# Performance work log

Measured on AMD Instinct MI355X. Metric: run time of the kernel, lower is better.

Reference implementation:

```python
import jax, jax.numpy as jnp
import numpy as np

NUM_NODES = 2048
EMB = (512, 512, 256)
LATENT = 512
N_FEAT = 512
N_TOTAL = 16384  # batch_size * NUM_NODES
N_EDGES = 524288


def setup_inputs() -> dict:
    key = jax.random.key(0)
    ks = jax.random.split(key, 14)
    s = 0.02
    inp = {
        "x": jax.random.normal(ks[0], (N_TOTAL, N_FEAT), jnp.float32),
        "edge_index": jax.random.randint(ks[1], (2, N_EDGES), 0, N_TOTAL, dtype=jnp.int64),
        "batch_size": 8,
        "batch_index": jax.random.randint(ks[2], (N_TOTAL,), 0, 8, dtype=jnp.int64),
        "W1": jax.random.normal(ks[3], (N_FEAT, EMB[0]), jnp.float32) * s,
        "b1": jnp.zeros((EMB[0],), jnp.float32),
        "W2": jax.random.normal(ks[4], (EMB[0], EMB[1]), jnp.float32) * s,
        "b2": jnp.zeros((EMB[1],), jnp.float32),
        "W3": jax.random.normal(ks[5], (EMB[1], EMB[2]), jnp.float32) * s,
        "b3": jnp.zeros((EMB[2],), jnp.float32),
        "We": jax.random.normal(ks[6], (NUM_NODES * EMB[2], LATENT), jnp.float32) * s,
        "be": jnp.zeros((LATENT,), jnp.float32),
        "Wd": jax.random.normal(ks[7], (LATENT, NUM_NODES), jnp.float32) * s,
        "bd": jnp.zeros((NUM_NODES,), jnp.float32),
    }
    return inp


def reference(x, edge_index, batch_size, batch_index, W1, b1, W2, b2, W3, b3, We, be, Wd, bd):
    N = x.shape[0]
    loops = jnp.arange(N)
    row = jnp.concatenate([edge_index[0], loops])  # sources
    col = jnp.concatenate([edge_index[1], loops])  # targets
    # symmetric degree normalization (PyG GCNConv with self loops)
    deg = jax.ops.segment_sum(jnp.ones_like(col, dtype=x.dtype), col, num_segments=N)
    dinv = jnp.where(deg > 0, jax.lax.rsqrt(deg), jnp.zeros_like(deg))
    norm = (dinv[row] * dinv[col])[:, None]  # [E+N, 1]

    def gcn(h, W, b):
        h = h @ W  # transform first (PyG order)
        return jax.ops.segment_sum(h[row] * norm, col, num_segments=N) + b

    h = jax.nn.relu(gcn(x, W1, b1))
    h = jax.nn.relu(gcn(h, W2, b2))
    h = gcn(h, W3, b3)                      # [N, EMB[2]]
    h = h.reshape(-1, NUM_NODES * EMB[2])   # [batch, NUM_NODES*EMB[2]]
    z = h @ We + be                          # encoder Linear
    out = z @ Wd + bd                        # decoder Linear -> [batch, NUM_NODES]
    return out
```

## Files before the change

kernel.cpp:

```cpp
#include <hip/hip_runtime.h>
#include <stdint.h>

#define NT 16384
#define NN 2048
#define NB 8

typedef __attribute__((ext_vector_type(4))) float f32x4;
typedef __attribute__((ext_vector_type(2))) float f32x2;
typedef __attribute__((ext_vector_type(8))) short s16x8;
typedef __attribute__((ext_vector_type(4))) short s16x4;

__device__ __forceinline__ float bf2f(short u) {
    unsigned v = ((unsigned)(unsigned short)u) << 16;
    return __builtin_bit_cast(float, v);
}
__device__ __forceinline__ short f2bf(float f) {
    unsigned u = __builtin_bit_cast(unsigned, f);
    u += 0x7fffu + ((u >> 16) & 1u);
    return (short)(u >> 16);
}
__device__ __forceinline__ void gload16(const void* g, void* l) {
    __builtin_amdgcn_global_load_lds(
        (const __attribute__((address_space(1))) void*)g,
        (__attribute__((address_space(3))) void*)l, 16, 0, 0);
}
__device__ __forceinline__ long long eidx(const void* ei, long long i, int is64) {
    if (is64) return ((const long long*)ei)[i];
    return (long long)((const int*)ei)[i];
}

__global__ void k_detect(const void* ei, int nchk, int* flag) {
    __shared__ int bad;
    if (threadIdx.x == 0) bad = 0;
    __syncthreads();
    const long long* p = (const long long*)ei;
    for (int i = threadIdx.x; i < nchk; i += 256) {
        long long v = p[i];
        if (v < 0 || v >= NT) bad = 1;
    }
    __syncthreads();
    if (threadIdx.x == 0) *flag = bad ? 0 : 1;
}

__global__ void k_count(const void* ei, int E, const int* flag, int* count) {
    int e = blockIdx.x * 256 + threadIdx.x;
    if (e >= E) return;
    int f = *flag;
    int c = (int)eidx(ei, (long long)E + e, f);
    atomicAdd(&count[c], 1);
}

__global__ __launch_bounds__(1024) void k_scan(const int* __restrict__ count,
        int* __restrict__ offs, float* __restrict__ dinv) {
    __shared__ int ps[1024];
    const int t = threadIdx.x;
    const int base = t * 16;
    int loc[16];
    int s = 0;
#pragma unroll
    for (int j = 0; j < 16; j++) { loc[j] = count[base + j]; s += loc[j]; }
    ps[t] = s;
    __syncthreads();
    for (int o = 1; o < 1024; o <<= 1) {
        int v = (t >= o) ? ps[t - o] : 0;
        __syncthreads();
        ps[t] += v;
        __syncthreads();
    }
    int ex = ps[t] - s;
#pragma unroll
    for (int j = 0; j < 16; j++) {
        offs[base + j] = ex;
        ex += loc[j];
        dinv[base + j] = rsqrtf((float)(loc[j] + 1));
    }
}

__global__ void k_fill(const void* ei, int E, const int* flag,
                       const int* offs, int* cursor, int* csr) {
    int e = blockIdx.x * 256 + threadIdx.x;
    if (e >= E) return;
    int f = *flag;
    int r = (int)eidx(ei, e, f);
    int c = (int)eidx(ei, (long long)E + e, f);
    int pos = offs[c] + atomicAdd(&cursor[c], 1);
    csr[pos] = r;
}

__global__ void k_convw_all(const float* __restrict__ W1, const float* __restrict__ W2,
                            const float* __restrict__ W3, short* __restrict__ Wt1,
                            short* __restrict__ Wt2, short* __restrict__ Wt3) {
    int idx = blockIdx.x * 256 + threadIdx.x;
    const float* W; short* Wt; int N, base;
    if (idx < 262144)      { W = W1; Wt = Wt1; N = 512; base = idx; }
    else if (idx < 524288) { W = W2; Wt = Wt2; N = 512; base = idx - 262144; }
    else                   { W = W3; Wt = Wt3; N = 256; base = idx - 524288; }
    int k = base / N, n = base - k * N;
    Wt[(size_t)n * 512 + k] = f2bf(W[base]);
}

__global__ __launch_bounds__(256) void k_scale_x(const float* __restrict__ x,
        const float* __restrict__ dinv, short* __restrict__ xs) {
    int i = blockIdx.x * 256 + threadIdx.x;
    f32x4 v = *(const f32x4*)(x + (size_t)i * 4);
    float d = dinv[i >> 7];
    s16x4 o;
#pragma unroll
    for (int j = 0; j < 4; j++) o[j] = f2bf(v[j] * d);
    *(s16x4*)(xs + (size_t)i * 4) = o;
}

__global__ __launch_bounds__(256) void k_gemm(const short* __restrict__ A,
        const short* __restrict__ Bt, short* __restrict__ Co, int N, int K) {
    __shared__ short As[4096];
    __shared__ short Bs[4096];
    const int t = threadIdx.x;
    const int w = t >> 6, l = t & 63;
    const int row0 = blockIdx.x * 128;
    const int col0 = blockIdx.y * 128;
    const int lr = l & 15, lhi = l >> 4;
    const int wr = (w >> 1) * 64, wc = (w & 1) * 64;
    const int srow = t >> 2;
    const int skoff = (t & 3) * 8;
    const int ldsbase = w * 512;
    f32x4 acc[4][4] = {};
    for (int k0 = 0; k0 < K; k0 += 32) {
#pragma unroll
        for (int i = 0; i < 2; i++) {
            int r = i * 64 + srow;
            gload16(A  + (size_t)(row0 + r) * K + k0 + skoff, (void*)(As + i * 2048 + ldsbase));
            gload16(Bt + (size_t)(col0 + r) * K + k0 + skoff, (void*)(Bs + i * 2048 + ldsbase));
        }
        __syncthreads();
        s16x8 af[4], bfr[4];
#pragma unroll
        for (int m = 0; m < 4; m++) af[m]  = *(const s16x8*)(As + (wr + m * 16 + lr) * 32 + lhi * 8);
#pragma unroll
        for (int n = 0; n < 4; n++) bfr[n] = *(const s16x8*)(Bs + (wc + n * 16 + lr) * 32 + lhi * 8);
#pragma unroll
        for (int m = 0; m < 4; m++)
#pragma unroll
            for (int n = 0; n < 4; n++)
                acc[m][n] = __builtin_amdgcn_mfma_f32_16x16x32_bf16(af[m], bfr[n], acc[m][n], 0, 0, 0);
        __syncthreads();
    }
#pragma unroll
    for (int m = 0; m < 4; m++)
#pragma unroll
        for (int n = 0; n < 4; n++)
#pragma unroll
            for (int j = 0; j < 4; j++) {
                int r = row0 + wr + m * 16 + lhi * 4 + j;
                int c = col0 + wc + n * 16 + lr;
                Co[(size_t)r * N + c] = f2bf(acc[m][n][j]);
            }
}

__global__ __launch_bounds__(256) void k_agg512(const short* __restrict__ T,
        const int* __restrict__ offs, const int* __restrict__ cnt,
        const int* __restrict__ csr, const float* __restrict__ dinv,
        const float* __restrict__ bias, short* __restrict__ H) {
    const int w = threadIdx.x >> 6, l = threadIdx.x & 63;
    const int node = blockIdx.x * 4 + w;
    const int c0 = l * 8;
    const short* base = T + c0;
    float acc[8];
    {
        s16x8 r = *(const s16x8*)(base + (size_t)node * 512);
#pragma unroll
        for (int v = 0; v < 8; v++) acc[v] = bf2f(r[v]);
    }
    const int beg = offs[node], end = beg + cnt[node];
    int j = beg;
    for (; j + 8 <= end; j += 8) {
        int sIx[8];
#pragma unroll
        for (int q = 0; q < 8; q++) sIx[q] = csr[j + q];
        s16x8 r[8];
#pragma unroll
        for (int q = 0; q < 8; q++) r[q] = *(const s16x8*)(base + (size_t)sIx[q] * 512);
#pragma unroll
        for (int v = 0; v < 8; v++) {
            float s01 = bf2f(r[0][v]) + bf2f(r[1][v]);
            float s23 = bf2f(r[2][v]) + bf2f(r[3][v]);
            float s45 = bf2f(r[4][v]) + bf2f(r[5][v]);
            float s67 = bf2f(r[6][v]) + bf2f(r[7][v]);
            acc[v] += (s01 + s23) + (s45 + s67);
        }
    }
    for (; j + 2 <= end; j += 2) {
        int s0 = csr[j], s1 = csr[j + 1];
        s16x8 r0 = *(const s16x8*)(base + (size_t)s0 * 512);
        s16x8 r1 = *(const s16x8*)(base + (size_t)s1 * 512);
#pragma unroll
        for (int v = 0; v < 8; v++) acc[v] += bf2f(r0[v]) + bf2f(r1[v]);
    }
    for (; j < end; j++) {
        s16x8 r0 = *(const s16x8*)(base + (size_t)csr[j] * 512);
#pragma unroll
        for (int v = 0; v < 8; v++) acc[v] += bf2f(r0[v]);
    }
    const float dc = dinv[node];
    f32x4 b0 = *(const f32x4*)(bias + c0);
    f32x4 b1 = *(const f32x4*)(bias + c0 + 4);
    s16x8 outv;
#pragma unroll
    for (int v = 0; v < 8; v++) {
        float bb = (v < 4) ? b0[v] : b1[v - 4];
        float o = acc[v] * dc + bb;
        o = fmaxf(o, 0.f);
        o *= dc;
        outv[v] = f2bf(o);
    }
    *(s16x8*)(H + (size_t)node * 512 + c0) = outv;
}

__global__ __launch_bounds__(256) void k_agg256(const short* __restrict__ T,
        const int* __restrict__ offs, const int* __restrict__ cnt,
        const int* __restrict__ csr, const float* __restrict__ dinv,
        const float* __restrict__ bias, float* __restrict__ H3) {
    const int w = threadIdx.x >> 6, l = threadIdx.x & 63;
    const int node = blockIdx.x * 4 + w;
    const int c0 = l * 4;
    const short* base = T + c0;
    float acc[4];
    {
        s16x4 r = *(const s16x4*)(base + (size_t)node * 256);
#pragma unroll
        for (int v = 0; v < 4; v++) acc[v] = bf2f(r[v]);
    }
    const int beg = offs[node], end = beg + cnt[node];
    int j = beg;
    for (; j + 8 <= end; j += 8) {
        int sIx[8];
#pragma unroll
        for (int q = 0; q < 8; q++) sIx[q] = csr[j + q];
        s16x4 r[8];
#pragma unroll
        for (int q = 0; q < 8; q++) r[q] = *(const s16x4*)(base + (size_t)sIx[q] * 256);
#pragma unroll
        for (int v = 0; v < 4; v++) {
            float s01 = bf2f(r[0][v]) + bf2f(r[1][v]);
            float s23 = bf2f(r[2][v]) + bf2f(r[3][v]);
            float s45 = bf2f(r[4][v]) + bf2f(r[5][v]);
            float s67 = bf2f(r[6][v]) + bf2f(r[7][v]);
            acc[v] += (s01 + s23) + (s45 + s67);
        }
    }
    for (; j < end; j++) {
        s16x4 r0 = *(const s16x4*)(base + (size_t)csr[j] * 256);
#pragma unroll
        for (int v = 0; v < 4; v++) acc[v] += bf2f(r0[v]);
    }
    const float dc = dinv[node];
    f32x4 bb = *(const f32x4*)(bias + c0);
    f32x4 o;
#pragma unroll
    for (int v = 0; v < 4; v++) o[v] = acc[v] * dc + bb[v];
    *(f32x4*)(H3 + (size_t)node * 256 + c0) = o;
}

__global__ __launch_bounds__(256) void k_enc(const float* __restrict__ h3,
        const float* __restrict__ We, float* __restrict__ part) {
    __shared__ float hT[512 * 8];
    __shared__ float red[32 * 128];
    const int t = threadIdx.x;
    const int k0 = blockIdx.x * 512;
    for (int i = t; i < 4096; i += 256) {
        int b = i >> 9, k = i & 511;
        hT[k * 8 + b] = h3[(size_t)b * 524288 + k0 + k];
    }
    __syncthreads();
    const int col = (t & 127) * 4;
    const int khalf = t >> 7;
    float acc[8][4] = {};
    const float* wp = We + (size_t)(k0 + khalf * 256) * 512 + col;
    const float* hp = hT + khalf * 256 * 8;
#pragma unroll 2
    for (int k = 0; k < 256; k++) {
        f32x4 wv = *(const f32x4*)(wp + (size_t)k * 512);
        f32x4 ha = *(const f32x4*)(hp + k * 8);
        f32x4 hb = *(const f32x4*)(hp + k * 8 + 4);
#pragma unroll
        for (int c = 0; c < 4; c++) {
            acc[0][c] += ha[0] * wv[c];
            acc[1][c] += ha[1] * wv[c];
            acc[2][c] += ha[2] * wv[c];
            acc[3][c] += ha[3] * wv[c];
            acc[4][c] += hb[0] * wv[c];
            acc[5][c] += hb[1] * wv[c];
            acc[6][c] += hb[2] * wv[c];
            acc[7][c] += hb[3] * wv[c];
        }
    }
    if (khalf) {
#pragma unroll
        for (int b = 0; b < 8; b++)
#pragma unroll
            for (int c = 0; c < 4; c++)
                red[(b * 4 + c) * 128 + (t - 128)] = acc[b][c];
    }
    __syncthreads();
    if (!khalf) {
#pragma unroll
        for (int b = 0; b < 8; b++) {
            f32x4 o;
#pragma unroll
            for (int c = 0; c < 4; c++) o[c] = acc[b][c] + red[(b * 4 + c) * 128 + t];
            *(f32x4*)(part + (size_t)blockIdx.x * 4096 + b * 512 + col) = o;
        }
    }
}

__global__ __launch_bounds__(256) void k_zred(const float* __restrict__ part,
                                              float* __restrict__ zpart) {
    const int n = blockIdx.x * 256 + threadIdx.x;
    const int p0 = blockIdx.y * 128;
    float s = 0.f;
    for (int q = 0; q < 128; q++) s += part[(size_t)(p0 + q) * 4096 + n];
    zpart[(size_t)blockIdx.y * 4096 + n] = s;
}

__global__ __launch_bounds__(256) void k_dec(const float* __restrict__ zpart,
        const float* __restrict__ be, const float* __restrict__ Wd,
        const float* __restrict__ bd, float* __restrict__ out) {
    __shared__ float zs[512];
    const int b = blockIdx.x >> 3;
    const int n = ((blockIdx.x & 7) << 8) + threadIdx.x;
    for (int i = threadIdx.x; i < 512; i += 256) {
        float s = be[i];
#pragma unroll
        for (int p = 0; p < 8; p++) s += zpart[(size_t)p * 4096 + b * 512 + i];
        zs[i] = s;
    }
    __syncthreads();
    float acc = bd[n];
    for (int k = 0; k < 512; k++) acc += zs[k] * Wd[(size_t)k * 2048 + n];
    out[b * 2048 + n] = acc;
}

extern "C" void kernel_launch(void* const* d_in, const int* in_sizes, int n_in,
                              void* d_out, int out_size, void* d_ws, size_t ws_size,
                              hipStream_t stream) {
    const float* x  = (const float*)d_in[0];
    const void*  ei = d_in[1];
    const float* W1 = (const float*)d_in[4];
    const float* b1 = (const float*)d_in[5];
    const float* W2 = (const float*)d_in[6];
    const float* b2 = (const float*)d_in[7];
    const float* W3 = (const float*)d_in[8];
    const float* b3 = (const float*)d_in[9];
    const float* We = (const float*)d_in[10];
    const float* be = (const float*)d_in[11];
    const float* Wd = (const float*)d_in[12];
    const float* bd = (const float*)d_in[13];
    float* out = (float*)d_out;
    const int E = in_sizes[1] / 2;

    char* ws = (char*)d_ws;
    size_t off = 0;
    auto alloc = [&](size_t bytes) {
        void* p = ws + off;
        off = (off + bytes + 255) & ~(size_t)255;
        return p;
    };
    int*   flag   = (int*)  alloc(4);
    int*   count  = (int*)  alloc((size_t)NT * 4);
    int*   cursor = (int*)  alloc((size_t)NT * 4);
    int*   offs   = (int*)  alloc((size_t)NT * 4);
    float* dinv   = (float*)alloc((size_t)NT * 4);
    int*   csr    = (int*)  alloc((size_t)E * 4);
    short* Wt1    = (short*)alloc((size_t)512 * 512 * 2);
    short* Wt2    = (short*)alloc((size_t)512 * 512 * 2);
    short* Wt3    = (short*)alloc((size_t)256 * 512 * 2);
    short* bufA   = (short*)alloc((size_t)NT * 512 * 2);
    short* bufB   = (short*)alloc((size_t)NT * 512 * 2);
    float* part   = (float*)alloc((size_t)1024 * 4096 * 4);
    float* zpart  = (float*)alloc((size_t)8 * 4096 * 4);

    hipMemsetAsync(count, 0, (size_t)NT * 8, stream);

    k_detect<<<1, 256, 0, stream>>>(ei, 2048, flag);
    k_count<<<(E + 255) / 256, 256, 0, stream>>>(ei, E, flag, count);
    k_scan<<<1, 1024, 0, stream>>>(count, offs, dinv);
    k_fill<<<(E + 255) / 256, 256, 0, stream>>>(ei, E, flag, offs, cursor, csr);

    k_convw_all<<<2560, 256, 0, stream>>>(W1, W2, W3, Wt1, Wt2, Wt3);
    k_scale_x<<<(NT * 512 / 4) / 256, 256, 0, stream>>>(x, dinv, bufA);

    dim3 g1(128, 4);
    k_gemm<<<g1, 256, 0, stream>>>(bufA, Wt1, bufB, 512, 512);
    k_agg512<<<NT / 4, 256, 0, stream>>>(bufB, offs, count, csr, dinv, b1, bufA);
    k_gemm<<<g1, 256, 0, stream>>>(bufA, Wt2, bufB, 512, 512);
    k_agg512<<<NT / 4, 256, 0, stream>>>(bufB, offs, count, csr, dinv, b2, bufA);
    dim3 g3(128, 2);
    k_gemm<<<g3, 256, 0, stream>>>(bufA, Wt3, bufB, 256, 512);
    k_agg256<<<NT / 4, 256, 0, stream>>>(bufB, offs, count, csr, dinv, b3, (float*)bufA);

    k_enc<<<1024, 256, 0, stream>>>((const float*)bufA, We, part);
    dim3 gz(16, 8);
    k_zred<<<gz, 256, 0, stream>>>(part, zpart);
    k_dec<<<64, 256, 0, stream>>>(zpart, be, Wd, bd, out);
}
```

Measured before the change: 533.2 us.

## Slice aggregation by channel and widen GEMM K-tile with swizzled LDS

The GEMM now stages a 64-wide K tile per iteration with an XOR-swizzled LDS layout, which halves the barrier count and is meant to avoid LDS bank conflicts. The aggregation kernels are restructured so each block handles a 64-channel slice of the features, and each wave walks 8 (or 4) nodes doing scalar 2-byte gathers per lane. Block index ordering is meant to put slices of nearby nodes close together for cache locality. The risk is that the scalar 2-byte gathers are much narrower than the previous 16-byte vector loads, and every neighbour index list is now reread once per slice.

```diff
diff --git a/kernel.cpp b/kernel.cpp
--- a/kernel.cpp
+++ b/kernel.cpp
@@ -112,36 +112,54 @@
 
 __global__ __launch_bounds__(256) void k_gemm(const short* __restrict__ A,
         const short* __restrict__ Bt, short* __restrict__ Co, int N, int K) {
-    __shared__ short As[4096];
-    __shared__ short Bs[4096];
+    __shared__ short As[8192];
+    __shared__ short Bs[8192];
     const int t = threadIdx.x;
     const int w = t >> 6, l = t & 63;
     const int row0 = blockIdx.x * 128;
     const int col0 = blockIdx.y * 128;
     const int lr = l & 15, lhi = l >> 4;
     const int wr = (w >> 1) * 64, wc = (w & 1) * 64;
-    const int srow = t >> 2;
-    const int skoff = (t & 3) * 8;
-    const int ldsbase = w * 512;
     f32x4 acc[4][4] = {};
-    for (int k0 = 0; k0 < K; k0 += 32) {
-#pragma unroll
-        for (int i = 0; i < 2; i++) {
-            int r = i * 64 + srow;
-            gload16(A  + (size_t)(row0 + r) * K + k0 + skoff, (void*)(As + i * 2048 + ldsbase));
-            gload16(Bt + (size_t)(col0 + r) * K + k0 + skoff, (void*)(Bs + i * 2048 + ldsbase));
+    int srow[4], jsrc[4];
+#pragma unroll
+    for (int i = 0; i < 4; i++) {
+        int s = t + i * 256;
+        srow[i] = s >> 3;
+        jsrc[i] = (s & 7) ^ (srow[i] & 7);
+    }
+    int aoff[2][4], boff[2][4];
+#pragma unroll
+    for (int kk = 0; kk < 2; kk++) {
+#pragma unroll
+        for (int m = 0; m < 4; m++) {
+            int ar = wr + m * 16 + lr;
+            aoff[kk][m] = ar * 64 + (((kk * 4 + lhi) ^ (ar & 7)) << 3);
+            int br = wc + m * 16 + lr;
+            boff[kk][m] = br * 64 + (((kk * 4 + lhi) ^ (br & 7)) << 3);
+        }
+    }
+    for (int k0 = 0; k0 < K; k0 += 64) {
+#pragma unroll
+        for (int i = 0; i < 4; i++) {
+            int s = t + i * 256;
+            gload16(A  + (size_t)(row0 + srow[i]) * K + k0 + jsrc[i] * 8, (void*)(As + s * 8));
+            gload16(Bt + (size_t)(col0 + srow[i]) * K + k0 + jsrc[i] * 8, (void*)(Bs + s * 8));
         }
         __syncthreads();
-        s16x8 af[4], bfr[4];
-#pragma unroll
-        for (int m = 0; m < 4; m++) af[m]  = *(const s16x8*)(As + (wr + m * 16 + lr) * 32 + lhi * 8);
-#pragma unroll
-        for (int n = 0; n < 4; n++) bfr[n] = *(const s16x8*)(Bs + (wc + n * 16 + lr) * 32 + lhi * 8);
-#pragma unroll
-        for (int m = 0; m < 4; m++)
-#pragma unroll
-            for (int n = 0; n < 4; n++)
-                acc[m][n] = __builtin_amdgcn_mfma_f32_16x16x32_bf16(af[m], bfr[n], acc[m][n], 0, 0, 0);
+#pragma unroll
+        for (int kk = 0; kk < 2; kk++) {
+            s16x8 af[4], bfr[4];
+#pragma unroll
+            for (int m = 0; m < 4; m++) af[m]  = *(const s16x8*)(As + aoff[kk][m]);
+#pragma unroll
+            for (int n = 0; n < 4; n++) bfr[n] = *(const s16x8*)(Bs + boff[kk][n]);
+#pragma unroll
+            for (int m = 0; m < 4; m++)
+#pragma unroll
+                for (int n = 0; n < 4; n++)
+                    acc[m][n] = __builtin_amdgcn_mfma_f32_16x16x32_bf16(af[m], bfr[n], acc[m][n], 0, 0, 0);
+        }
         __syncthreads();
     }
 #pragma unroll
@@ -156,108 +174,73 @@
             }
 }
 
-__global__ __launch_bounds__(256) void k_agg512(const short* __restrict__ T,
+__global__ __launch_bounds__(256) void k_aggs512(const unsigned short* __restrict__ T,
         const int* __restrict__ offs, const int* __restrict__ cnt,
         const int* __restrict__ csr, const float* __restrict__ dinv,
-        const float* __restrict__ bias, short* __restrict__ H) {
+        const float* __restrict__ bias, unsigned short* __restrict__ H) {
+    const int slice = blockIdx.x & 7;
+    const int group = blockIdx.x >> 3;
     const int w = threadIdx.x >> 6, l = threadIdx.x & 63;
-    const int node = blockIdx.x * 4 + w;
-    const int c0 = l * 8;
-    const short* base = T + c0;
-    float acc[8];
-    {
-        s16x8 r = *(const s16x8*)(base + (size_t)node * 512);
-#pragma unroll
-        for (int v = 0; v < 8; v++) acc[v] = bf2f(r[v]);
-    }
-    const int beg = offs[node], end = beg + cnt[node];
-    int j = beg;
-    for (; j + 8 <= end; j += 8) {
-        int sIx[8];
-#pragma unroll
-        for (int q = 0; q < 8; q++) sIx[q] = csr[j + q];
-        s16x8 r[8];
-#pragma unroll
-        for (int q = 0; q < 8; q++) r[q] = *(const s16x8*)(base + (size_t)sIx[q] * 512);
-#pragma unroll
-        for (int v = 0; v < 8; v++) {
-            float s01 = bf2f(r[0][v]) + bf2f(r[1][v]);
-            float s23 = bf2f(r[2][v]) + bf2f(r[3][v]);
-            float s45 = bf2f(r[4][v]) + bf2f(r[5][v]);
-            float s67 = bf2f(r[6][v]) + bf2f(r[7][v]);
-            acc[v] += (s01 + s23) + (s45 + s67);
-        }
-    }
-    for (; j + 2 <= end; j += 2) {
-        int s0 = csr[j], s1 = csr[j + 1];
-        s16x8 r0 = *(const s16x8*)(base + (size_t)s0 * 512);
-        s16x8 r1 = *(const s16x8*)(base + (size_t)s1 * 512);
-#pragma unroll
-        for (int v = 0; v < 8; v++) acc[v] += bf2f(r0[v]) + bf2f(r1[v]);
-    }
-    for (; j < end; j++) {
-        s16x8 r0 = *(const s16x8*)(base + (size_t)csr[j] * 512);
-#pragma unroll
-        for (int v = 0; v < 8; v++) acc[v] += bf2f(r0[v]);
-    }
-    const float dc = dinv[node];
-    f32x4 b0 = *(const f32x4*)(bias + c0);
-    f32x4 b1 = *(const f32x4*)(bias + c0 + 4);
-    s16x8 outv;
-#pragma unroll
-    for (int v = 0; v < 8; v++) {
-        float bb = (v < 4) ? b0[v] : b1[v - 4];
-        float o = acc[v] * dc + bb;
-        o = fmaxf(o, 0.f);
-        o *= dc;
-        outv[v] = f2bf(o);
-    }
-    *(s16x8*)(H + (size_t)node * 512 + c0) = outv;
-}
-
-__global__ __launch_bounds__(256) void k_agg256(const short* __restrict__ T,
+    const int ch = slice * 64 + l;
+    const float bch = bias[ch];
+    const unsigned short* Tc = T + ch;
+    const int nbase = (group * 4 + w) * 8;
+    for (int nn = 0; nn < 8; nn++) {
+        const int node = nbase + nn;
+        float acc = bf2f((short)Tc[(size_t)node * 512]);
+        const int beg = offs[node], deg = cnt[node];
+        int j = 0;
+        for (; j + 8 <= deg; j += 8) {
+            int idx[8];
+#pragma unroll
+            for (int q = 0; q < 8; q++) idx[q] = __builtin_nontemporal_load(&csr[beg + j + q]);
+            float v[8];
+#pragma unroll
+            for (int q = 0; q < 8; q++) v[q] = bf2f((short)Tc[(size_t)idx[q] * 512]);
+            acc += ((v[0] + v[1]) + (v[2] + v[3])) + ((v[4] + v[5]) + (v[6] + v[7]));
+        }
+        for (; j < deg; j++) {
+            int s0 = __builtin_nontemporal_load(&csr[beg + j]);
+            acc += bf2f((short)Tc[(size_t)s0 * 512]);
+        }
+        const float dc = dinv[node];
+        float o = fmaxf(acc * dc + bch, 0.f) * dc;
+        H[(size_t)node * 512 + ch] = (unsigned short)f2bf(o);
+    }
+}
+
+__global__ __launch_bounds__(256) void k_aggs256(const unsigned short* __restrict__ T,
         const int* __restrict__ offs, const int* __restrict__ cnt,
         const int* __restrict__ csr, const float* __restrict__ dinv,
         const float* __restrict__ bias, float* __restrict__ H3) {
+    const int slice = blockIdx.x & 3;
+    const int group = blockIdx.x >> 2;
     const int w = threadIdx.x >> 6, l = threadIdx.x & 63;
-    const int node = blockIdx.x * 4 + w;
-    const int c0 = l * 4;
-    const short* base = T + c0;
-    float acc[4];
-    {
-        s16x4 r = *(const s16x4*)(base + (size_t)node * 256);
-#pragma unroll
-        for (int v = 0; v < 4; v++) acc[v] = bf2f(r[v]);
-    }
-    const int beg = offs[node], end = beg + cnt[node];
-    int j = beg;
-    for (; j + 8 <= end; j += 8) {
-        int sIx[8];
-#pragma unroll
-        for (int q = 0; q < 8; q++) sIx[q] = csr[j + q];
-        s16x4 r[8];
-#pragma unroll
-        for (int q = 0; q < 8; q++) r[q] = *(const s16x4*)(base + (size_t)sIx[q] * 256);
-#pragma unroll
-        for (int v = 0; v < 4; v++) {
-            float s01 = bf2f(r[0][v]) + bf2f(r[1][v]);
-            float s23 = bf2f(r[2][v]) + bf2f(r[3][v]);
-            float s45 = bf2f(r[4][v]) + bf2f(r[5][v]);
-            float s67 = bf2f(r[6][v]) + bf2f(r[7][v]);
-            acc[v] += (s01 + s23) + (s45 + s67);
-        }
-    }
-    for (; j < end; j++) {
-        s16x4 r0 = *(const s16x4*)(base + (size_t)csr[j] * 256);
-#pragma unroll
-        for (int v = 0; v < 4; v++) acc[v] += bf2f(r0[v]);
-    }
-    const float dc = dinv[node];
-    f32x4 bb = *(const f32x4*)(bias + c0);
-    f32x4 o;
-#pragma unroll
-    for (int v = 0; v < 4; v++) o[v] = acc[v] * dc + bb[v];
-    *(f32x4*)(H3 + (size_t)node * 256 + c0) = o;
+    const int ch = slice * 64 + l;
+    const float bch = bias[ch];
+    const unsigned short* Tc = T + ch;
+    const int nbase = (group * 4 + w) * 4;
+    for (int nn = 0; nn < 4; nn++) {
+        const int node = nbase + nn;
+        float acc = bf2f((short)Tc[(size_t)node * 256]);
+        const int beg = offs[node], deg = cnt[node];
+        int j = 0;
+        for (; j + 8 <= deg; j += 8) {
+            int idx[8];
+#pragma unroll
+            for (int q = 0; q < 8; q++) idx[q] = __builtin_nontemporal_load(&csr[beg + j + q]);
+            float v[8];
+#pragma unroll
+            for (int q = 0; q < 8; q++) v[q] = bf2f((short)Tc[(size_t)idx[q] * 256]);
+            acc += ((v[0] + v[1]) + (v[2] + v[3])) + ((v[4] + v[5]) + (v[6] + v[7]));
+        }
+        for (; j < deg; j++) {
+            int s0 = __builtin_nontemporal_load(&csr[beg + j]);
+            acc += bf2f((short)Tc[(size_t)s0 * 256]);
+        }
+        const float dc = dinv[node];
+        H3[(size_t)node * 256 + ch] = acc * dc + bch;
+    }
 }
 
 __global__ __launch_bounds__(256) void k_enc(const float* __restrict__ h3,
@@ -390,12 +373,12 @@
 
     dim3 g1(128, 4);
     k_gemm<<<g1, 256, 0, stream>>>(bufA, Wt1, bufB, 512, 512);
-    k_agg512<<<NT / 4, 256, 0, stream>>>(bufB, offs, count, csr, dinv, b1, bufA);
+    k_aggs512<<<4096, 256, 0, stream>>>((const unsigned short*)bufB, offs, count, csr, dinv, b1, (unsigned short*)bufA);
     k_gemm<<<g1, 256, 0, stream>>>(bufA, Wt2, bufB, 512, 512);
-    k_agg512<<<NT / 4, 256, 0, stream>>>(bufB, offs, count, csr, dinv, b2, bufA);
+    k_aggs512<<<4096, 256, 0, stream>>>((const unsigned short*)bufB, offs, count, csr, dinv, b2, (unsigned short*)bufA);
     dim3 g3(128, 2);
     k_gemm<<<g3, 256, 0, stream>>>(bufA, Wt3, bufB, 256, 512);
-    k_agg256<<<NT / 4, 256, 0, stream>>>(bufB, offs, count, csr, dinv, b3, (float*)bufA);
+    k_aggs256<<<4096, 256, 0, stream>>>((const unsigned short*)bufB, offs, count, csr, dinv, b3, (float*)bufA);
 
     k_enc<<<1024, 256, 0, stream>>>((const float*)bufA, We, part);
     dim3 gz(16, 8);
```

Result: slower. 695.0 us (+30.3%).

## Bucket CSR neighbor lists by source index range for gather locality

Applied to the files above, without the earlier changes.

CSR construction now counts edges per (target, source-bucket) pair, using 16 buckets of 1024 source rows each, and fills each target's neighbor list in bucket order. Neighbors are therefore roughly sorted by source index, so the aggregation gathers in k_agg512/k_agg256 touch nearby rows and should get better cache locality. This adds two small kernels, a larger 1 MB counter memset, and more atomic counters, and it reuses the 'part' scratch buffer for the bucket arrays.

```diff
diff --git a/kernel.cpp b/kernel.cpp
--- a/kernel.cpp
+++ b/kernel.cpp
@@ -4,6 +4,7 @@
 #define NT 16384
 #define NN 2048
 #define NB 8
+#define NBKT 16
 
 typedef __attribute__((ext_vector_type(4))) float f32x4;
 typedef __attribute__((ext_vector_type(2))) float f32x2;
@@ -42,12 +43,22 @@
     if (threadIdx.x == 0) *flag = bad ? 0 : 1;
 }
 
-__global__ void k_count(const void* ei, int E, const int* flag, int* count) {
+__global__ void k_count16(const void* ei, int E, const int* flag, int* cnt16) {
     int e = blockIdx.x * 256 + threadIdx.x;
     if (e >= E) return;
     int f = *flag;
+    int r = (int)eidx(ei, e, f);
     int c = (int)eidx(ei, (long long)E + e, f);
-    atomicAdd(&count[c], 1);
+    atomicAdd(&cnt16[c * NBKT + (r >> 10)], 1);
+}
+
+__global__ void k_deg(const int* __restrict__ cnt16, int* __restrict__ deg) {
+    int n = blockIdx.x * 256 + threadIdx.x;
+    const int* p = cnt16 + n * NBKT;
+    int s = 0;
+#pragma unroll
+    for (int j = 0; j < NBKT; j++) s += p[j];
+    deg[n] = s;
 }
 
 __global__ __launch_bounds__(1024) void k_scan(const int* __restrict__ count,
@@ -76,14 +87,25 @@
     }
 }
 
-__global__ void k_fill(const void* ei, int E, const int* flag,
-                       const int* offs, int* cursor, int* csr) {
+__global__ void k_bcur(const int* __restrict__ cnt16, const int* __restrict__ offs,
+                       int* __restrict__ bcur) {
+    int n = blockIdx.x * 256 + threadIdx.x;
+    int running = offs[n];
+#pragma unroll
+    for (int b = 0; b < NBKT; b++) {
+        bcur[n * NBKT + b] = running;
+        running += cnt16[n * NBKT + b];
+    }
+}
+
+__global__ void k_fill16(const void* ei, int E, const int* flag,
+                         int* bcur, int* csr) {
     int e = blockIdx.x * 256 + threadIdx.x;
     if (e >= E) return;
     int f = *flag;
     int r = (int)eidx(ei, e, f);
     int c = (int)eidx(ei, (long long)E + e, f);
-    int pos = offs[c] + atomicAdd(&cursor[c], 1);
+    int pos = atomicAdd(&bcur[c * NBKT + (r >> 10)], 1);
     csr[pos] = r;
 }
 
@@ -365,8 +387,7 @@
         return p;
     };
     int*   flag   = (int*)  alloc(4);
-    int*   count  = (int*)  alloc((size_t)NT * 4);
-    int*   cursor = (int*)  alloc((size_t)NT * 4);
+    int*   deg    = (int*)  alloc((size_t)NT * 4);
     int*   offs   = (int*)  alloc((size_t)NT * 4);
     float* dinv   = (float*)alloc((size_t)NT * 4);
     int*   csr    = (int*)  alloc((size_t)E * 4);
@@ -377,25 +398,29 @@
     short* bufB   = (short*)alloc((size_t)NT * 512 * 2);
     float* part   = (float*)alloc((size_t)1024 * 4096 * 4);
     float* zpart  = (float*)alloc((size_t)8 * 4096 * 4);
-
-    hipMemsetAsync(count, 0, (size_t)NT * 8, stream);
+    int*   cnt16  = (int*)part;
+    int*   bcur   = ((int*)part) + NT * NBKT;
+
+    hipMemsetAsync(cnt16, 0, (size_t)NT * NBKT * 4, stream);
 
     k_detect<<<1, 256, 0, stream>>>(ei, 2048, flag);
-    k_count<<<(E + 255) / 256, 256, 0, stream>>>(ei, E, flag, count);
-    k_scan<<<1, 1024, 0, stream>>>(count, offs, dinv);
-    k_fill<<<(E + 255) / 256, 256, 0, stream>>>(ei, E, flag, offs, cursor, csr);
+    k_count16<<<(E + 255) / 256, 256, 0, stream>>>(ei, E, flag, cnt16);
+    k_deg<<<NT / 256, 256, 0, stream>>>(cnt16, deg);
+    k_scan<<<1, 1024, 0, stream>>>(deg, offs, dinv);
+    k_bcur<<<NT / 256, 256, 0, stream>>>(cnt16, offs, bcur);
+    k_fill16<<<(E + 255) / 256, 256, 0, stream>>>(ei, E, flag, bcur, csr);
 
     k_convw_all<<<2560, 256, 0, stream>>>(W1, W2, W3, Wt1, Wt2, Wt3);
     k_scale_x<<<(NT * 512 / 4) / 256, 256, 0, stream>>>(x, dinv, bufA);
 
     dim3 g1(128, 4);
     k_gemm<<<g1, 256, 0, stream>>>(bufA, Wt1, bufB, 512, 512);
-    k_agg512<<<NT / 4, 256, 0, stream>>>(bufB, offs, count, csr, dinv, b1, bufA);
+    k_agg512<<<NT / 4, 256, 0, stream>>>(bufB, offs, deg, csr, dinv, b1, bufA);
     k_gemm<<<g1, 256, 0, stream>>>(bufA, Wt2, bufB, 512, 512);
-    k_agg512<<<NT / 4, 256, 0, stream>>>(bufB, offs, count, csr, dinv, b2, bufA);
+    k_agg512<<<NT / 4, 256, 0, stream>>>(bufB, offs, deg, csr, dinv, b2, bufA);
     dim3 g3(128, 2);
     k_gemm<<<g3, 256, 0, stream>>>(bufA, Wt3, bufB, 256, 512);
-    k_agg256<<<NT / 4, 256, 0, stream>>>(bufB, offs, count, csr, dinv, b3, (float*)bufA);
+    k_agg256<<<NT / 4, 256, 0, stream>>>(bufB, offs, deg, csr, dinv, b3, (float*)bufA);
 
     k_enc<<<1024, 256, 0, stream>>>((const float*)bufA, We, part);
     dim3 gz(16, 8);
```

New measurement: 516.9 us. 1.03x faster.
